# Kernel tuning notes

Measured on AMD Instinct MI355X. Metric: run time of the kernel, lower is better.

## Reference

```python
import jax, jax.numpy as jnp
import numpy as np

NA, NPAP = 50000, 100000
D_IN, D_HID, D_OUT = 512, 512, 256
E_AP, E_PA, E_AA = 400000, 400000, 200000
NEG_SLOPE = 0.2


def setup_inputs() -> dict:
    key = jax.random.key(0)
    ks = jax.random.split(key, 18)
    f32 = jnp.float32

    def edges(k, e, n_src, n_dst):
        k1, k2 = jax.random.split(k)
        return jnp.stack([
            jax.random.randint(k1, (e,), 0, n_src),
            jax.random.randint(k2, (e,), 0, n_dst),
        ]).astype(jnp.int64)

    return {
        'x_author': jax.random.normal(ks[0], (NA, D_IN), f32),
        'x_paper': jax.random.normal(ks[1], (NPAP, D_IN), f32),
        # layer 1 params
        'W1': jax.random.normal(ks[2], (2, D_IN, D_HID), f32) / np.sqrt(D_IN),
        'b1': jnp.zeros((2, D_HID), f32),
        'att1': jax.random.normal(ks[3], (3, 2, D_HID), f32) * 0.1,
        'kW1': jax.random.normal(ks[4], (D_HID, D_HID), f32) / np.sqrt(D_HID),
        'kb1': jnp.zeros((D_HID,), f32),
        'q1': jax.random.normal(ks[5], (D_HID,), f32) * 0.1,
        # layer 2 params
        'W2': jax.random.normal(ks[6], (2, D_HID, D_OUT), f32) / np.sqrt(D_HID),
        'b2': jnp.zeros((2, D_OUT), f32),
        'att2': jax.random.normal(ks[7], (3, 2, D_OUT), f32) * 0.1,
        'kW2': jax.random.normal(ks[8], (D_OUT, D_OUT), f32) / np.sqrt(D_OUT),
        'kb2': jnp.zeros((D_OUT,), f32),
        'q2': jax.random.normal(ks[9], (D_OUT,), f32) * 0.1,
        # edge index dict: (author,writes,paper), (paper,written_by,author), (author,coauthor,author)
        'e_ap': edges(ks[10], E_AP, NA, NPAP),
        'e_pa': edges(ks[11], E_PA, NPAP, NA),
        'e_aa': edges(ks[12], E_AA, NA, NA),
    }


def _edge_type_attn(h_src, h_dst, a_src, a_dst, ei, n_dst):
    """One edge-type GAT-style aggregation of HANConv (heads=1)."""
    src, dst = ei[0], ei[1]
    alpha = (h_src @ a_src)[src] + (h_dst @ a_dst)[dst]        # [E]
    alpha = jax.nn.leaky_relu(alpha, NEG_SLOPE)
    m = jax.ops.segment_max(alpha, dst, num_segments=n_dst)    # softmax over dst groups
    e = jnp.exp(alpha - m[dst])
    denom = jax.ops.segment_sum(e, dst, num_segments=n_dst)
    w = e / denom[dst]                                          # [E]
    out = jax.ops.segment_sum(h_src[src] * w[:, None], dst, num_segments=n_dst)
    return jax.nn.relu(out)                                     # [n_dst, D]


def _semantic_group(outs, kW, kb, q):
    """outs: [T, N, D]; semantic attention over T metapaths."""
    score = jnp.einsum('tnd,d->t', jnp.tanh(outs @ kW + kb), q) / outs.shape[1]
    attn = jax.nn.softmax(score)
    return jnp.einsum('t,tnd->nd', attn, outs)


def _han_layer(x_a, x_p, W, b, att, kW, kb, q, e_ap, e_pa, e_aa):
    h_a = x_a @ W[0] + b[0]   # per-node-type projection
    h_p = x_p @ W[1] + b[1]
    na, npap = h_a.shape[0], h_p.shape[0]
    out_p = _edge_type_attn(h_a, h_p, att[0, 0], att[0, 1], e_ap, npap)
    out_a1 = _edge_type_attn(h_p, h_a, att[1, 0], att[1, 1], e_pa, na)
    out_a2 = _edge_type_attn(h_a, h_a, att[2, 0], att[2, 1], e_aa, na)
    out_a = _semantic_group(jnp.stack([out_a1, out_a2]), kW, kb, q)
    out_p = _semantic_group(out_p[None], kW, kb, q)
    return out_a, out_p


def reference(x_author, x_paper, W1, b1, att1, kW1, kb1, q1,
              W2, b2, att2, kW2, kb2, q2, e_ap, e_pa, e_aa):
    h_a, h_p = _han_layer(x_author, x_paper, W1, b1, att1, kW1, kb1, q1, e_ap, e_pa, e_aa)
    h_a, h_p = _han_layer(h_a, h_p, W2, b2, att2, kW2, kb2, q2, e_ap, e_pa, e_aa)
    return h_a  # x['author']
```

## Files before the change

kernel.cpp:

```cpp
#include <hip/hip_runtime.h>
#include <hip/hip_bf16.h>

#define NA 50000
#define NPAP 100000
#define DIN 512
#define DHID 512
#define DOUT 256
#define EAP 400000
#define EPA 400000
#define EAA 200000

typedef unsigned short u16;
typedef __attribute__((ext_vector_type(8))) short bf16x8;
typedef __attribute__((ext_vector_type(4))) float f32x4;

__device__ inline float bflo(unsigned v) { return __uint_as_float(v << 16); }
__device__ inline float bfhi(unsigned v) { return __uint_as_float(v & 0xffff0000u); }
__device__ inline u16 f2bf_rne(float x) {
    unsigned u = __float_as_uint(x);
    return (u16)((u + 0x7FFFu + ((u >> 16) & 1u)) >> 16);
}
__device__ inline unsigned pack2bf(float a, float b) {
    return (unsigned)f2bf_rne(a) | ((unsigned)f2bf_rne(b) << 16);
}


__global__ void fill_u32_kernel(unsigned* __restrict__ p, unsigned v, int n) {
    int i = blockIdx.x * blockDim.x + threadIdx.x;
    if (i < n) p[i] = v;
}

__global__ void detect_kernel(const unsigned* __restrict__ e, int npairs, int* __restrict__ flag) {
    __shared__ int anyn;
    if (threadIdx.x == 0) anyn = 0;
    __syncthreads();
    unsigned local = 0;
    for (int i = threadIdx.x; i < npairs; i += blockDim.x) local |= e[2 * i + 1];
    if (local) atomicOr(&anyn, 1);
    __syncthreads();
    if (threadIdx.x == 0) flag[0] = (anyn == 0) ? 1 : 0;
}

__device__ inline int edge_at(const void* e, size_t idx, int i64) {
    return i64 ? (int)((const long long*)e)[idx] : ((const int*)e)[idx];
}


__global__ void conv_bt_kernel(const float* __restrict__ B, u16* __restrict__ bth,
                               u16* __restrict__ btl, int K, int N) {
    __shared__ float tile[32][33];
    const int nb = blockIdx.x * 32, kb = blockIdx.y * 32;
    const int tx = threadIdx.x, ty = threadIdx.y;
    const int KBLK = K >> 5;
    for (int i = ty; i < 32; i += 8)
        tile[i][tx] = B[(size_t)(kb + i) * N + nb + tx];
    __syncthreads();
    for (int i = ty; i < 32; i += 8) {
        float v = tile[tx][i];
        unsigned u = __float_as_uint(v);
        unsigned h = (u + 0x7FFFu + ((u >> 16) & 1u)) >> 16;
        float hf = __uint_as_float(h << 16);
        float r = v - hf;
        unsigned l = __float_as_uint(r) >> 16;
        const int n = nb + i, k = kb + tx;
        const int nblk = n >> 7, row = n & 127;
        const int kblk = k >> 5, kc = (k & 31) >> 3, ke = k & 7;
        const int cph = kc ^ ((row >> 1) & 3);
        size_t o = (((size_t)(nblk * KBLK + kblk) * 128 + row) << 5) + (cph << 3) + ke;
        bth[o] = (u16)h;
        btl[o] = (u16)l;
    }
}


template <bool BF16OUT>
__global__ __launch_bounds__(256, 4) void mfma_gemm_2p_kernel(
    const float* __restrict__ A,
    const u16* __restrict__ Bth, const u16* __restrict__ Btl,
    const float* __restrict__ bias,
    float* __restrict__ C, int M, int N, int K, int gx)
{
    __shared__ u16 Ah[128][32];
    __shared__ u16 Bh[128][32];
    __shared__ u16 Bl[128][32];

    const int nwg = gridDim.x;
    const int bid = blockIdx.x;
    const int qc = nwg >> 3, rc = nwg & 7;
    const int xcd = bid & 7, idx = bid >> 3;
    const int wg = (xcd < rc ? xcd * (qc + 1) : rc * (qc + 1) + (xcd - rc) * qc) + idx;
    const int bx = wg % gx, by = wg / gx;
    const int m0 = by * 128;
    const int n0 = bx * 128;

    const int tid = threadIdx.x;
    const int lane = tid & 63;
    const int wv = tid >> 6;
    const int wm = wv >> 1, wn = wv & 1;
    const int fr = lane & 15;
    const int kg = lane >> 4;

    const int srow = tid >> 1;
    const int oh   = tid & 1;
    const bool a_ok = (m0 + srow) < M;
    const float* Ap = A + (size_t)(m0 + srow) * K + oh * 16;

    const int swc = (srow >> 1) & 3;
    const int p0 = srow * 32 + ((((oh << 1) + 0) ^ swc) << 3);
    const int p1 = srow * 32 + ((((oh << 1) + 1) ^ swc) << 3);
    const int rdc = (kg ^ ((fr >> 1) & 3)) << 3;

    const int KBLK = K >> 5;
    const size_t btile0 = ((size_t)(n0 >> 7) * KBLK) << 12;
    const int bso0 = wv * 512 + lane * 8;
    const int bso1 = (wv + 4) * 512 + lane * 8;

    f32x4 acc[4][4] = {};

    const int nt = K >> 5;
    for (int t = 0; t < nt; ++t) {
        __syncthreads();
        {
            const int k0 = t << 5;
            uint4 w0 = make_uint4(0, 0, 0, 0), w1 = w0;
            if (a_ok) {
                float ar[16];
#pragma unroll
                for (int c4 = 0; c4 < 4; ++c4) {
                    float4 v = *(const float4*)(Ap + k0 + c4 * 4);
                    ar[c4 * 4 + 0] = v.x; ar[c4 * 4 + 1] = v.y;
                    ar[c4 * 4 + 2] = v.z; ar[c4 * 4 + 3] = v.w;
                }
                w0 = make_uint4(pack2bf(ar[0], ar[1]), pack2bf(ar[2], ar[3]),
                                pack2bf(ar[4], ar[5]), pack2bf(ar[6], ar[7]));
                w1 = make_uint4(pack2bf(ar[8], ar[9]), pack2bf(ar[10], ar[11]),
                                pack2bf(ar[12], ar[13]), pack2bf(ar[14], ar[15]));
            }
            const u16* bt = Bth + btile0 + ((size_t)t << 12);
            const u16* blt = Btl + btile0 + ((size_t)t << 12);
            uint4 bh0 = *(const uint4*)(bt + bso0);
            uint4 bh1 = *(const uint4*)(bt + bso1);
            uint4 bl0 = *(const uint4*)(blt + bso0);
            uint4 bl1 = *(const uint4*)(blt + bso1);

            u16* ahp = &Ah[0][0];
            *(uint4*)&ahp[p0] = w0;
            *(uint4*)&ahp[p1] = w1;
            u16* bhp = &Bh[0][0];
            u16* blp = &Bl[0][0];
            *(uint4*)&bhp[bso0] = bh0;
            *(uint4*)&bhp[bso1] = bh1;
            *(uint4*)&blp[bso0] = bl0;
            *(uint4*)&blp[bso1] = bl1;
        }
        __syncthreads();

        bf16x8 afh[4], bfh[4], bfl[4];
#pragma unroll
        for (int i = 0; i < 4; ++i) {
            const int aoff = (wm * 64 + i * 16 + fr) * 32 + rdc;
            const int boff = (wn * 64 + i * 16 + fr) * 32 + rdc;
            afh[i] = *(const bf16x8*)&Ah[0][aoff];
            bfh[i] = *(const bf16x8*)&Bh[0][boff];
            bfl[i] = *(const bf16x8*)&Bl[0][boff];
        }
#pragma unroll
        for (int i = 0; i < 4; ++i)
#pragma unroll
            for (int j = 0; j < 4; ++j) {
                acc[i][j] = __builtin_amdgcn_mfma_f32_16x16x32_bf16(afh[i], bfh[j], acc[i][j], 0, 0, 0);
                acc[i][j] = __builtin_amdgcn_mfma_f32_16x16x32_bf16(afh[i], bfl[j], acc[i][j], 0, 0, 0);
            }
    }

#pragma unroll
    for (int j = 0; j < 4; ++j) {
        const int col = n0 + wn * 64 + j * 16 + fr;
        const float bj = bias[col];
#pragma unroll
        for (int i = 0; i < 4; ++i) {
            const int rbase = m0 + wm * 64 + i * 16 + kg * 4;
#pragma unroll
            for (int r = 0; r < 4; ++r) {
                const int grow = rbase + r;
                if (grow < M) {
                    if (BF16OUT)
                        ((u16*)C)[(size_t)grow * N + col] = f2bf_rne(acc[i][j][r] + bj);
                    else
                        C[(size_t)grow * N + col] = acc[i][j][r] + bj;
                }
            }
        }
    }
}


template <bool COMB>
__global__ __launch_bounds__(256, 4) void mfma_gemm_bfA_kernel(
    const u16* __restrict__ A, const u16* __restrict__ A2,
    const float* __restrict__ cwp,
    const u16* __restrict__ Bth, const u16* __restrict__ Btl,
    const float* __restrict__ bias,
    float* __restrict__ C, int M, int N, int K, int gx)
{
    __shared__ u16 Ah[128][32];
    __shared__ u16 Bh[128][32];
    __shared__ u16 Bl[128][32];

    const int nwg = gridDim.x;
    const int bid = blockIdx.x;
    const int qc = nwg >> 3, rc = nwg & 7;
    const int xcd = bid & 7, idx = bid >> 3;
    const int wg = (xcd < rc ? xcd * (qc + 1) : rc * (qc + 1) + (xcd - rc) * qc) + idx;
    const int bx = wg % gx, by = wg / gx;
    const int m0 = by * 128;
    const int n0 = bx * 128;

    const int tid = threadIdx.x;
    const int lane = tid & 63;
    const int wv = tid >> 6;
    const int wm = wv >> 1, wn = wv & 1;
    const int fr = lane & 15;
    const int kg = lane >> 4;

    const int srow = tid >> 1;
    const int oh   = tid & 1;
    const bool a_ok = (m0 + srow) < M;
    const u16* Ap  = A + (size_t)(m0 + srow) * K + oh * 16;
    const u16* Ap2 = COMB ? (A2 + (size_t)(m0 + srow) * K + oh * 16) : nullptr;
    float cw0 = 1.f, cw1 = 0.f;
    if (COMB) { cw0 = cwp[0]; cw1 = cwp[1]; }

    const int swc = (srow >> 1) & 3;
    const int p0 = srow * 32 + ((((oh << 1) + 0) ^ swc) << 3);
    const int p1 = srow * 32 + ((((oh << 1) + 1) ^ swc) << 3);
    const int rdc = (kg ^ ((fr >> 1) & 3)) << 3;

    const int KBLK = K >> 5;
    const size_t btile0 = ((size_t)(n0 >> 7) * KBLK) << 12;
    const int bso0 = wv * 512 + lane * 8;
    const int bso1 = (wv + 4) * 512 + lane * 8;

    f32x4 acc[4][4] = {};

    const int nt = K >> 5;
    for (int t = 0; t < nt; ++t) {
        __syncthreads();
        {
            const int k0 = t << 5;
            uint4 a0 = make_uint4(0, 0, 0, 0), a1 = a0;
            if (a_ok) {
                a0 = *(const uint4*)(Ap + k0);
                a1 = *(const uint4*)(Ap + k0 + 8);
                if (COMB) {
                    uint4 c0 = *(const uint4*)(Ap2 + k0);
                    uint4 c1 = *(const uint4*)(Ap2 + k0 + 8);
                    a0.x = pack2bf(cw0 * bflo(a0.x) + cw1 * bflo(c0.x), cw0 * bfhi(a0.x) + cw1 * bfhi(c0.x));
                    a0.y = pack2bf(cw0 * bflo(a0.y) + cw1 * bflo(c0.y), cw0 * bfhi(a0.y) + cw1 * bfhi(c0.y));
                    a0.z = pack2bf(cw0 * bflo(a0.z) + cw1 * bflo(c0.z), cw0 * bfhi(a0.z) + cw1 * bfhi(c0.z));
                    a0.w = pack2bf(cw0 * bflo(a0.w) + cw1 * bflo(c0.w), cw0 * bfhi(a0.w) + cw1 * bfhi(c0.w));
                    a1.x = pack2bf(cw0 * bflo(a1.x) + cw1 * bflo(c1.x), cw0 * bfhi(a1.x) + cw1 * bfhi(c1.x));
                    a1.y = pack2bf(cw0 * bflo(a1.y) + cw1 * bflo(c1.y), cw0 * bfhi(a1.y) + cw1 * bfhi(c1.y));
                    a1.z = pack2bf(cw0 * bflo(a1.z) + cw1 * bflo(c1.z), cw0 * bfhi(a1.z) + cw1 * bfhi(c1.z));
                    a1.w = pack2bf(cw0 * bflo(a1.w) + cw1 * bflo(c1.w), cw0 * bfhi(a1.w) + cw1 * bfhi(c1.w));
                }
            }
            const u16* bt = Bth + btile0 + ((size_t)t << 12);
            const u16* blt = Btl + btile0 + ((size_t)t << 12);
            uint4 bh0 = *(const uint4*)(bt + bso0);
            uint4 bh1 = *(const uint4*)(bt + bso1);
            uint4 bl0 = *(const uint4*)(blt + bso0);
            uint4 bl1 = *(const uint4*)(blt + bso1);

            u16* ahp = &Ah[0][0];
            *(uint4*)&ahp[p0] = a0;
            *(uint4*)&ahp[p1] = a1;
            u16* bhp = &Bh[0][0];
            u16* blp = &Bl[0][0];
            *(uint4*)&bhp[bso0] = bh0;
            *(uint4*)&bhp[bso1] = bh1;
            *(uint4*)&blp[bso0] = bl0;
            *(uint4*)&blp[bso1] = bl1;
        }
        __syncthreads();

        bf16x8 afh[4], bfh[4], bfl[4];
#pragma unroll
        for (int i = 0; i < 4; ++i) {
            const int aoff = (wm * 64 + i * 16 + fr) * 32 + rdc;
            const int boff = (wn * 64 + i * 16 + fr) * 32 + rdc;
            afh[i] = *(const bf16x8*)&Ah[0][aoff];
            bfh[i] = *(const bf16x8*)&Bh[0][boff];
            bfl[i] = *(const bf16x8*)&Bl[0][boff];
        }
#pragma unroll
        for (int i = 0; i < 4; ++i)
#pragma unroll
            for (int j = 0; j < 4; ++j) {
                acc[i][j] = __builtin_amdgcn_mfma_f32_16x16x32_bf16(afh[i], bfh[j], acc[i][j], 0, 0, 0);
                acc[i][j] = __builtin_amdgcn_mfma_f32_16x16x32_bf16(afh[i], bfl[j], acc[i][j], 0, 0, 0);
            }
    }

#pragma unroll
    for (int j = 0; j < 4; ++j) {
        const int col = n0 + wn * 64 + j * 16 + fr;
        const float bj = bias[col];
#pragma unroll
        for (int i = 0; i < 4; ++i) {
            const int rbase = m0 + wm * 64 + i * 16 + kg * 4;
#pragma unroll
            for (int r = 0; r < 4; ++r) {
                const int grow = rbase + r;
                if (grow < M) C[(size_t)grow * N + col] = acc[i][j][r] + bj;
            }
        }
    }
}


template <bool BF16A>
__global__ __launch_bounds__(256, 4) void mfma_score1_kernel(
    const void* __restrict__ A_, const u16* __restrict__ Bth,
    const float* __restrict__ bias, int M, int N, int K,
    const float* __restrict__ qv, float* __restrict__ score, int gx)
{
    __shared__ u16 Ah[128][32];
    __shared__ u16 Bh[128][32];

    const int nwg = gridDim.x;
    const int bid = blockIdx.x;
    const int qc = nwg >> 3, rc = nwg & 7;
    const int xcd = bid & 7, idx = bid >> 3;
    const int wg = (xcd < rc ? xcd * (qc + 1) : rc * (qc + 1) + (xcd - rc) * qc) + idx;
    const int bx = wg % gx, by = wg / gx;
    const int m0 = by * 128;
    const int n0 = bx * 128;

    const int tid = threadIdx.x;
    const int lane = tid & 63;
    const int wv = tid >> 6;
    const int wm = wv >> 1, wn = wv & 1;
    const int fr = lane & 15;
    const int kg = lane >> 4;

    const int srow = tid >> 1;
    const int oh   = tid & 1;
    const bool a_ok = (m0 + srow) < M;

    const int swc = (srow >> 1) & 3;
    const int p0 = srow * 32 + ((((oh << 1) + 0) ^ swc) << 3);
    const int p1 = srow * 32 + ((((oh << 1) + 1) ^ swc) << 3);
    const int rdc = (kg ^ ((fr >> 1) & 3)) << 3;

    const int KBLK = K >> 5;
    const size_t btile0 = ((size_t)(n0 >> 7) * KBLK) << 12;
    const int bso0 = wv * 512 + lane * 8;
    const int bso1 = (wv + 4) * 512 + lane * 8;

    f32x4 acc[4][4] = {};

    const int nt = K >> 5;
    for (int t = 0; t < nt; ++t) {
        __syncthreads();
        {
            const int k0 = t << 5;
            uint4 w0 = make_uint4(0, 0, 0, 0), w1 = w0;
            if (a_ok) {
                if (BF16A) {
                    const u16* Ap = (const u16*)A_ + (size_t)(m0 + srow) * K + oh * 16;
                    w0 = *(const uint4*)(Ap + k0);
                    w1 = *(const uint4*)(Ap + k0 + 8);
                } else {
                    const float* Ap = (const float*)A_ + (size_t)(m0 + srow) * K + oh * 16;
                    float ar[16];
#pragma unroll
                    for (int c4 = 0; c4 < 4; ++c4) {
                        float4 v = *(const float4*)(Ap + k0 + c4 * 4);
                        ar[c4 * 4 + 0] = v.x; ar[c4 * 4 + 1] = v.y;
                        ar[c4 * 4 + 2] = v.z; ar[c4 * 4 + 3] = v.w;
                    }
                    w0 = make_uint4(pack2bf(ar[0], ar[1]), pack2bf(ar[2], ar[3]),
                                    pack2bf(ar[4], ar[5]), pack2bf(ar[6], ar[7]));
                    w1 = make_uint4(pack2bf(ar[8], ar[9]), pack2bf(ar[10], ar[11]),
                                    pack2bf(ar[12], ar[13]), pack2bf(ar[14], ar[15]));
                }
            }
            const u16* bt = Bth + btile0 + ((size_t)t << 12);
            uint4 bh0 = *(const uint4*)(bt + bso0);
            uint4 bh1 = *(const uint4*)(bt + bso1);
            u16* ahp = &Ah[0][0];
            *(uint4*)&ahp[p0] = w0;
            *(uint4*)&ahp[p1] = w1;
            u16* bhp = &Bh[0][0];
            *(uint4*)&bhp[bso0] = bh0;
            *(uint4*)&bhp[bso1] = bh1;
        }
        __syncthreads();

        bf16x8 afh[4], bfh[4];
#pragma unroll
        for (int i = 0; i < 4; ++i) {
            afh[i] = *(const bf16x8*)&Ah[0][(wm * 64 + i * 16 + fr) * 32 + rdc];
            bfh[i] = *(const bf16x8*)&Bh[0][(wn * 64 + i * 16 + fr) * 32 + rdc];
        }
#pragma unroll
        for (int i = 0; i < 4; ++i)
#pragma unroll
            for (int j = 0; j < 4; ++j)
                acc[i][j] = __builtin_amdgcn_mfma_f32_16x16x32_bf16(afh[i], bfh[j], acc[i][j], 0, 0, 0);
    }

    float ssum = 0.f;
#pragma unroll
    for (int j = 0; j < 4; ++j) {
        const int col = n0 + wn * 64 + j * 16 + fr;
        const float bj = bias[col];
        const float qj = qv[col];
#pragma unroll
        for (int i = 0; i < 4; ++i) {
            const int rbase = m0 + wm * 64 + i * 16 + kg * 4;
#pragma unroll
            for (int r = 0; r < 4; ++r) {
                if (rbase + r < M) ssum += tanhf(acc[i][j][r] + bj) * qj;
            }
        }
    }
#pragma unroll
    for (int o = 32; o; o >>= 1) ssum += __shfl_xor(ssum, o);
    __syncthreads();
    float* red = (float*)&Ah[0][0];
    if (lane == 0) red[wv] = ssum;
    __syncthreads();
    if (tid == 0) atomicAdd(score, red[0] + red[1] + red[2] + red[3]);
}


template <int NV, bool BF16IN>
__global__ void scores_kernel(const void* __restrict__ h, int n, int D,
                              const float* __restrict__ v0, const float* __restrict__ v1,
                              const float* __restrict__ v2, const float* __restrict__ v3,
                              float* __restrict__ s0, float* __restrict__ s1,
                              float* __restrict__ s2, float* __restrict__ s3)
{
    const int lane = threadIdx.x & 63;
    int wid = (blockIdx.x * blockDim.x + threadIdx.x) >> 6;
    const int nw = (gridDim.x * blockDim.x) >> 6;
    for (int node = wid; node < n; node += nw) {
        float a0 = 0, a1 = 0, a2 = 0, a3 = 0;
        for (int d = lane * 4; d < D; d += 256) {
            float4 x;
            if (BF16IN) {
                const u16* row = (const u16*)h + (size_t)node * D;
                uint2 bv = *(const uint2*)&row[d];
                x = make_float4(bflo(bv.x), bfhi(bv.x), bflo(bv.y), bfhi(bv.y));
            } else {
                const float* row = (const float*)h + (size_t)node * D;
                x = *(const float4*)&row[d];
            }
            float4 w = *(const float4*)&v0[d];
            a0 += x.x * w.x + x.y * w.y + x.z * w.z + x.w * w.w;
            if (NV > 1) { float4 u = *(const float4*)&v1[d]; a1 += x.x * u.x + x.y * u.y + x.z * u.z + x.w * u.w; }
            if (NV > 2) { float4 u = *(const float4*)&v2[d]; a2 += x.x * u.x + x.y * u.y + x.z * u.z + x.w * u.w; }
            if (NV > 3) { float4 u = *(const float4*)&v3[d]; a3 += x.x * u.x + x.y * u.y + x.z * u.z + x.w * u.w; }
        }
#pragma unroll
        for (int o = 32; o; o >>= 1) {
            a0 += __shfl_xor(a0, o);
            if (NV > 1) a1 += __shfl_xor(a1, o);
            if (NV > 2) a2 += __shfl_xor(a2, o);
            if (NV > 3) a3 += __shfl_xor(a3, o);
        }
        if (lane == 0) {
            s0[node] = a0;
            if (NV > 1) s1[node] = a1;
            if (NV > 2) s2[node] = a2;
            if (NV > 3) s3[node] = a3;
        }
    }
}


__global__ void count3_kernel(const void* __restrict__ eA, const void* __restrict__ eB,
                              const void* __restrict__ eC, const int* __restrict__ flag,
                              int* __restrict__ cA, int* __restrict__ cB, int* __restrict__ cC) {
    int i = blockIdx.x * blockDim.x + threadIdx.x;
    int f = *flag;
    if (i < EAP) {
        atomicAdd(&cA[edge_at(eA, (size_t)EAP + i, f)], 1);
    } else if (i < EAP + EPA) {
        int j = i - EAP;
        atomicAdd(&cB[edge_at(eB, (size_t)EPA + j, f)], 1);
    } else if (i < EAP + EPA + EAA) {
        int j = i - EAP - EPA;
        atomicAdd(&cC[edge_at(eC, (size_t)EAA + j, f)], 1);
    }
}

__global__ void scan3_kernel(int* __restrict__ c0, int n0_, int* __restrict__ o0, int* __restrict__ u0,
                             int* __restrict__ c1, int n1_, int* __restrict__ o1, int* __restrict__ u1,
                             int* __restrict__ c2, int n2_, int* __restrict__ o2, int* __restrict__ u2) {
    const int b = blockIdx.x;
    int* cnt   = b == 0 ? c0 : (b == 1 ? c1 : c2);
    const int n = b == 0 ? n0_ : (b == 1 ? n1_ : n2_);
    int* offs  = b == 0 ? o0 : (b == 1 ? o1 : o2);
    int* cur   = b == 0 ? u0 : (b == 1 ? u1 : u2);
    __shared__ int wsum[16];
    __shared__ int carry_s;
    const int t = threadIdx.x;
    const int lane = t & 63, w = t >> 6;
    if (t == 0) carry_s = 0;
    __syncthreads();
    for (int base = 0; base < n; base += 1024) {
        int v = (base + t < n) ? cnt[base + t] : 0;
        int x = v;
#pragma unroll
        for (int o = 1; o < 64; o <<= 1) {
            int y = __shfl_up(x, o);
            if (lane >= o) x += y;
        }
        if (lane == 63) wsum[w] = x;
        __syncthreads();
        if (w == 0 && lane < 16) {
            int s = wsum[lane];
#pragma unroll
            for (int o = 1; o < 16; o <<= 1) {
                int y = __shfl_up(s, o);
                if (lane >= o) s += y;
            }
            wsum[lane] = s;
        }
        __syncthreads();
        const int carry = carry_s;
        const int woff = (w > 0) ? wsum[w - 1] : 0;
        if (base + t < n) {
            int excl = carry + woff + x - v;
            offs[base + t] = excl;
            cur[base + t] = excl;
        }
        __syncthreads();
        if (t == 1023) carry_s = carry + wsum[15];
        __syncthreads();
    }
    if (t == 0) offs[n] = carry_s;
}

__global__ void scatter3_kernel(const void* __restrict__ eA, const void* __restrict__ eB,
                                const void* __restrict__ eC, const int* __restrict__ flag,
                                int* __restrict__ uA, int* __restrict__ uB, int* __restrict__ uC,
                                int* __restrict__ idA, int* __restrict__ idB, int* __restrict__ idC) {
    int i = blockIdx.x * blockDim.x + threadIdx.x;
    int f = *flag;
    if (i < EAP) {
        int d = edge_at(eA, (size_t)EAP + i, f);
        idA[atomicAdd(&uA[d], 1)] = i;
    } else if (i < EAP + EPA) {
        int j = i - EAP;
        int d = edge_at(eB, (size_t)EPA + j, f);
        idB[atomicAdd(&uB[d], 1)] = j;
    } else if (i < EAP + EPA + EAA) {
        int j = i - EAP - EPA;
        int d = edge_at(eC, (size_t)EAA + j, f);
        idC[atomicAdd(&uC[d], 1)] = j;
    }
}


template <int DW, bool BF16H, bool BF16OUT>
__global__ __launch_bounds__(256) void agg_fused_kernel(
    const int* __restrict__ offs, const int* __restrict__ eids,
    const void* __restrict__ e, const int* __restrict__ flag,
    const float* __restrict__ ssrc, const float* __restrict__ sdst,
    const void* __restrict__ hsrc_, void* __restrict__ out,
    int n_dst, int E, int D)
{
    const int lane = threadIdx.x & 63;
    int wid = (blockIdx.x * blockDim.x + threadIdx.x) >> 6;
    const int nw = (gridDim.x * blockDim.x) >> 6;
    const int f = *flag;
    for (int dst = wid; dst < n_dst; dst += nw) {
        const int beg = offs[dst], end = offs[dst + 1];
        const float sd = sdst[dst];

        float dsum = 0.f;
        for (int j = beg + lane; j < end; j += 64) {
            int eid = eids[j];
            float a = ssrc[edge_at(e, eid, f)] + sd;
            a = (a >= 0.f) ? a : 0.2f * a;
            dsum += expf(a);
        }
#pragma unroll
        for (int o = 32; o; o >>= 1) dsum += __shfl_xor(dsum, o);
        const float rden = (end > beg) ? 1.f / dsum : 0.f;

        float acc[DW] = {};
        int j = beg;
        for (; j + 4 <= end; j += 4) {
            const int e0 = eids[j], e1 = eids[j + 1], e2 = eids[j + 2], e3 = eids[j + 3];
            const int q0 = edge_at(e, e0, f), q1 = edge_at(e, e1, f);
            const int q2 = edge_at(e, e2, f), q3 = edge_at(e, e3, f);
            float a0 = ssrc[q0] + sd, a1 = ssrc[q1] + sd;
            float a2 = ssrc[q2] + sd, a3 = ssrc[q3] + sd;
            a0 = (a0 >= 0.f) ? a0 : 0.2f * a0;
            a1 = (a1 >= 0.f) ? a1 : 0.2f * a1;
            a2 = (a2 >= 0.f) ? a2 : 0.2f * a2;
            a3 = (a3 >= 0.f) ? a3 : 0.2f * a3;
            const float w0 = expf(a0) * rden, w1 = expf(a1) * rden;
            const float w2 = expf(a2) * rden, w3 = expf(a3) * rden;
            if (BF16H) {
                const u16* hb = (const u16*)hsrc_;
                const u16* r0 = hb + (size_t)q0 * D + lane * DW;
                const u16* r1 = hb + (size_t)q1 * D + lane * DW;
                const u16* r2 = hb + (size_t)q2 * D + lane * DW;
                const u16* r3 = hb + (size_t)q3 * D + lane * DW;
#pragma unroll
                for (int c = 0; c < DW; c += 8) {
                    uint4 b0 = *(const uint4*)&r0[c];
                    uint4 b1 = *(const uint4*)&r1[c];
                    uint4 b2 = *(const uint4*)&r2[c];
                    uint4 b3 = *(const uint4*)&r3[c];
                    acc[c + 0] += bflo(b0.x) * w0 + bflo(b1.x) * w1 + bflo(b2.x) * w2 + bflo(b3.x) * w3;
                    acc[c + 1] += bfhi(b0.x) * w0 + bfhi(b1.x) * w1 + bfhi(b2.x) * w2 + bfhi(b3.x) * w3;
                    acc[c + 2] += bflo(b0.y) * w0 + bflo(b1.y) * w1 + bflo(b2.y) * w2 + bflo(b3.y) * w3;
                    acc[c + 3] += bfhi(b0.y) * w0 + bfhi(b1.y) * w1 + bfhi(b2.y) * w2 + bfhi(b3.y) * w3;
                    acc[c + 4] += bflo(b0.z) * w0 + bflo(b1.z) * w1 + bflo(b2.z) * w2 + bflo(b3.z) * w3;
                    acc[c + 5] += bfhi(b0.z) * w0 + bfhi(b1.z) * w1 + bfhi(b2.z) * w2 + bfhi(b3.z) * w3;
                    acc[c + 6] += bflo(b0.w) * w0 + bflo(b1.w) * w1 + bflo(b2.w) * w2 + bflo(b3.w) * w3;
                    acc[c + 7] += bfhi(b0.w) * w0 + bfhi(b1.w) * w1 + bfhi(b2.w) * w2 + bfhi(b3.w) * w3;
                }
            } else {
                const float* hf = (const float*)hsrc_;
                const float* r0 = hf + (size_t)q0 * D + lane * DW;
                const float* r1 = hf + (size_t)q1 * D + lane * DW;
                const float* r2 = hf + (size_t)q2 * D + lane * DW;
                const float* r3 = hf + (size_t)q3 * D + lane * DW;
#pragma unroll
                for (int c = 0; c < DW; c += 4) {
                    float4 a0v = *(const float4*)&r0[c];
                    float4 a1v = *(const float4*)&r1[c];
                    float4 a2v = *(const float4*)&r2[c];
                    float4 a3v = *(const float4*)&r3[c];
                    acc[c + 0] += a0v.x * w0 + a1v.x * w1 + a2v.x * w2 + a3v.x * w3;
                    acc[c + 1] += a0v.y * w0 + a1v.y * w1 + a2v.y * w2 + a3v.y * w3;
                    acc[c + 2] += a0v.z * w0 + a1v.z * w1 + a2v.z * w2 + a3v.z * w3;
                    acc[c + 3] += a0v.w * w0 + a1v.w * w1 + a2v.w * w2 + a3v.w * w3;
                }
            }
        }
        for (; j < end; ++j) {
            const int eid = eids[j];
            const int q = edge_at(e, eid, f);
            float a = ssrc[q] + sd;
            a = (a >= 0.f) ? a : 0.2f * a;
            const float w = expf(a) * rden;
            if (BF16H) {
                const u16* row = (const u16*)hsrc_ + (size_t)q * D + lane * DW;
#pragma unroll
                for (int c = 0; c < DW; c += 8) {
                    uint4 b0 = *(const uint4*)&row[c];
                    acc[c + 0] += bflo(b0.x) * w; acc[c + 1] += bfhi(b0.x) * w;
                    acc[c + 2] += bflo(b0.y) * w; acc[c + 3] += bfhi(b0.y) * w;
                    acc[c + 4] += bflo(b0.z) * w; acc[c + 5] += bfhi(b0.z) * w;
                    acc[c + 6] += bflo(b0.w) * w; acc[c + 7] += bfhi(b0.w) * w;
                }
            } else {
                const float* row = (const float*)hsrc_ + (size_t)q * D + lane * DW;
#pragma unroll
                for (int c = 0; c < DW; c += 4) {
                    float4 v = *(const float4*)&row[c];
                    acc[c + 0] += v.x * w; acc[c + 1] += v.y * w;
                    acc[c + 2] += v.z * w; acc[c + 3] += v.w * w;
                }
            }
        }
        if (BF16OUT) {
            u16* orow = (u16*)out + (size_t)dst * D + lane * DW;
#pragma unroll
            for (int c = 0; c < DW; c += 8) {
                uint4 v;
                v.x = pack2bf(fmaxf(acc[c + 0], 0.f), fmaxf(acc[c + 1], 0.f));
                v.y = pack2bf(fmaxf(acc[c + 2], 0.f), fmaxf(acc[c + 3], 0.f));
                v.z = pack2bf(fmaxf(acc[c + 4], 0.f), fmaxf(acc[c + 5], 0.f));
                v.w = pack2bf(fmaxf(acc[c + 6], 0.f), fmaxf(acc[c + 7], 0.f));
                *(uint4*)&orow[c] = v;
            }
        } else {
            float* orow = (float*)out + (size_t)dst * D + lane * DW;
#pragma unroll
            for (int c = 0; c < DW; c += 4) {
                float4 v = make_float4(fmaxf(acc[c + 0], 0.f), fmaxf(acc[c + 1], 0.f),
                                       fmaxf(acc[c + 2], 0.f), fmaxf(acc[c + 3], 0.f));
                *(float4*)&orow[c] = v;
            }
        }
    }
}


__global__ void softmax2_kernel(const float* __restrict__ score, float invN, float* __restrict__ w) {
    if (threadIdx.x == 0 && blockIdx.x == 0) {
        float s0 = score[0] * invN, s1 = score[1] * invN;
        float m = fmaxf(s0, s1);
        float e0 = expf(s0 - m), e1 = expf(s1 - m);
        float r = 1.f / (e0 + e1);
        w[0] = e0 * r;
        w[1] = e1 * r;
    }
}

__global__ void combine2_kernel(const float4* __restrict__ a, const float4* __restrict__ b,
                                const float* __restrict__ w, float4* __restrict__ o, int n4) {
    float w0 = w[0], w1 = w[1];
    for (int i = blockIdx.x * blockDim.x + threadIdx.x; i < n4; i += gridDim.x * blockDim.x) {
        float4 x = a[i], y = b[i];
        o[i] = make_float4(w0 * x.x + w1 * y.x, w0 * x.y + w1 * y.y,
                           w0 * x.z + w1 * y.z, w0 * x.w + w1 * y.w);
    }
}


extern "C" void kernel_launch(void* const* d_in, const int* in_sizes, int n_in,
                              void* d_out, int out_size, void* d_ws, size_t ws_size,
                              hipStream_t stream) {
    const float* x_a  = (const float*)d_in[0];
    const float* x_p  = (const float*)d_in[1];
    const float* W1   = (const float*)d_in[2];
    const float* b1   = (const float*)d_in[3];
    const float* att1 = (const float*)d_in[4];
    const float* kW1  = (const float*)d_in[5];
    const float* kb1  = (const float*)d_in[6];
    const float* q1   = (const float*)d_in[7];
    const float* W2   = (const float*)d_in[8];
    const float* b2   = (const float*)d_in[9];
    const float* att2 = (const float*)d_in[10];
    const float* kW2  = (const float*)d_in[11];
    const float* kb2  = (const float*)d_in[12];
    const float* q2   = (const float*)d_in[13];
    const void* e_ap  = d_in[14];
    const void* e_pa  = d_in[15];
    const void* e_aa  = d_in[16];
    float* out = (float*)d_out;

    size_t off = 0;
    auto ALLOC = [&](size_t nbytes) -> void* {
        void* p = (char*)d_ws + off;
        off += (nbytes + 255) & ~(size_t)255;
        return p;
    };
    float* bufA = (float*)ALLOC((size_t)NPAP * DHID * 4);
    float* bufB = (float*)ALLOC((size_t)NA * DHID * 4);
    float* bufC = (float*)ALLOC((size_t)NA * DHID * 4);
    float* bufD = (float*)ALLOC((size_t)NA * DHID * 4);
    float* sa_w  = (float*)ALLOC((size_t)NA * 4);
    float* sa_pd = (float*)ALLOC((size_t)NA * 4);
    float* sa_as = (float*)ALLOC((size_t)NA * 4);
    float* sa_ad = (float*)ALLOC((size_t)NA * 4);
    float* sp_wd = (float*)ALLOC((size_t)NPAP * 4);
    float* sp_ps = (float*)ALLOC((size_t)NPAP * 4);
    int* cnt3    = (int*)ALLOC((size_t)(NPAP + 2 * NA + 8) * 4);
    int* cursor3 = (int*)ALLOC((size_t)(NPAP + 2 * NA + 8) * 4);
    int* offs_ap = (int*)ALLOC((size_t)(NPAP + 1) * 4);
    int* offs_pa = (int*)ALLOC((size_t)(NA + 1) * 4);
    int* offs_aa = (int*)ALLOC((size_t)(NA + 1) * 4);
    int* eids_ap = (int*)ALLOC((size_t)EAP * 4);
    int* eids_pa = (int*)ALLOC((size_t)EPA * 4);
    int* eids_aa = (int*)ALLOC((size_t)EAA * 4);
    const size_t WTOT = 262144u * 3 + 131072u * 2 + 65536u;
    u16* w_hi = (u16*)ALLOC(WTOT * 2);
    u16* w_lo = (u16*)ALLOC(WTOT * 2);
    float* score = (float*)ALLOC(8 * 4);
    float* wsem  = (float*)ALLOC(2 * 4);
    int* eflag   = (int*)ALLOC(4);
    if (off > ws_size) return;

    const size_t oW1a = 0, oW1p = 262144, okW1 = 524288;
    const size_t oW2a = 786432, oW2p = 917504, okW2 = 1048576;

    int* cntA = cnt3;                 int* curA = cursor3;
    int* cntB = cnt3 + NPAP + 1;      int* curB = cursor3 + NPAP + 1;
    int* cntC = cntB + NA + 1;        int* curC = curB + NA + 1;
    const int CNT3N = NPAP + 2 * NA + 3;

    hipStream_t s = stream;

    detect_kernel<<<1, 256, 0, s>>>((const unsigned*)e_ap, 1024, eflag);

    auto conv_b = [&](const float* B_, int K, int N, size_t wo) {
        conv_bt_kernel<<<dim3(N / 32, K / 32), dim3(32, 8), 0, s>>>(B_, w_hi + wo, w_lo + wo, K, N);
    };
    conv_b(W1, DIN, DHID, oW1a);
    conv_b(W1 + (size_t)DIN * DHID, DIN, DHID, oW1p);
    conv_b(kW1, DHID, DHID, okW1);
    conv_b(W2, DHID, DOUT, oW2a);
    conv_b(W2 + (size_t)DHID * DOUT, DHID, DOUT, oW2p);
    conv_b(kW2, DOUT, DOUT, okW2);

    {
        const int ETOT = EAP + EPA + EAA;
        fill_u32_kernel<<<(CNT3N + 255) / 256, 256, 0, s>>>((unsigned*)cnt3, 0u, CNT3N);
        count3_kernel<<<(ETOT + 255) / 256, 256, 0, s>>>(e_ap, e_pa, e_aa, eflag, cntA, cntB, cntC);
        scan3_kernel<<<3, 1024, 0, s>>>(cntA, NPAP, offs_ap, curA,
                                        cntB, NA, offs_pa, curB,
                                        cntC, NA, offs_aa, curC);
        scatter3_kernel<<<(ETOT + 255) / 256, 256, 0, s>>>(e_ap, e_pa, e_aa, eflag,
                                                           curA, curB, curC,
                                                           eids_ap, eids_pa, eids_aa);
    }

    auto gemm_proj_h = [&](const float* A_, size_t wo, const float* bias_, float* C_,
                           int M, int N, int K) {
        int gx = N / 128;
        int nwg = gx * ((M + 127) / 128);
        mfma_gemm_2p_kernel<true><<<nwg, 256, 0, s>>>(A_,
            w_hi + wo, w_lo + wo, bias_, C_, M, N, K, gx);
    };
    auto gemm_proj_bfA = [&](const u16* A_, size_t wo, const float* bias_, float* C_,
                             int M, int N, int K) {
        int gx = N / 128;
        int nwg = gx * ((M + 127) / 128);
        mfma_gemm_bfA_kernel<false><<<nwg, 256, 0, s>>>(A_, nullptr, nullptr,
            w_hi + wo, w_lo + wo, bias_, C_, M, N, K, gx);
    };
    auto gemm_proj_bfA_comb = [&](const u16* A_, const u16* A2_, const float* cw, size_t wo,
                                  const float* bias_, float* C_, int M, int N, int K) {
        int gx = N / 128;
        int nwg = gx * ((M + 127) / 128);
        mfma_gemm_bfA_kernel<true><<<nwg, 256, 0, s>>>(A_, A2_, cw,
            w_hi + wo, w_lo + wo, bias_, C_, M, N, K, gx);
    };
    auto gemm_score_b = [&](const void* A_, size_t wo, const float* bias_, int M, int N, int K,
                            const float* qv, float* sc) {
        int gx = N / 128;
        int nwg = gx * ((M + 127) / 128);
        mfma_score1_kernel<true><<<nwg, 256, 0, s>>>(A_, w_hi + wo, bias_, M, N, K, qv, sc, gx);
    };
    auto gemm_score_f = [&](const void* A_, size_t wo, const float* bias_, int M, int N, int K,
                            const float* qv, float* sc) {
        int gx = N / 128;
        int nwg = gx * ((M + 127) / 128);
        mfma_score1_kernel<false><<<nwg, 256, 0, s>>>(A_, w_hi + wo, bias_, M, N, K, qv, sc, gx);
    };

    u16* h_a = (u16*)bufB;
    u16* h_p = (u16*)bufA;
    gemm_proj_h(x_a, oW1a, b1, (float*)h_a, NA, DHID, DIN);
    gemm_proj_h(x_p, oW1p, b1 + DHID, (float*)h_p, NPAP, DHID, DIN);

    {
        int ga = (NA + 3) / 4 < 4096 ? (NA + 3) / 4 : 4096;
        int gp = (NPAP + 3) / 4 < 4096 ? (NPAP + 3) / 4 : 4096;
        scores_kernel<4, true><<<ga, 256, 0, s>>>(h_a, NA, DHID,
            att1 + 0 * DHID, att1 + 3 * DHID, att1 + 4 * DHID, att1 + 5 * DHID,
            sa_w, sa_pd, sa_as, sa_ad);
        scores_kernel<2, true><<<gp, 256, 0, s>>>(h_p, NPAP, DHID,
            att1 + 1 * DHID, att1 + 2 * DHID, nullptr, nullptr,
            sp_wd, sp_ps, nullptr, nullptr);
    }

    u16* o1  = (u16*)bufC;
    u16* o2  = (u16*)bufD;
    u16* x2p = (u16*)bufA + (size_t)NPAP * DHID;
    {
        int gw = (NA + 3) / 4;
        agg_fused_kernel<8, true, true><<<gw, 256, 0, s>>>(offs_pa, eids_pa, e_pa, eflag,
            sp_ps, sa_pd, h_p, o1, NA, EPA, DHID);
        agg_fused_kernel<8, true, true><<<gw, 256, 0, s>>>(offs_aa, eids_aa, e_aa, eflag,
            sa_as, sa_ad, h_a, o2, NA, EAA, DHID);
        int gw2 = (NPAP + 3) / 4;
        agg_fused_kernel<8, true, true><<<gw2, 256, 0, s>>>(offs_ap, eids_ap, e_ap, eflag,
            sa_w, sp_wd, h_a, x2p, NPAP, EAP, DHID);
    }

    fill_u32_kernel<<<1, 64, 0, s>>>((unsigned*)score, 0u, 2);
    gemm_score_b(o1, okW1, kb1, NA, DHID, DHID, q1, &score[0]);
    gemm_score_b(o2, okW1, kb1, NA, DHID, DHID, q1, &score[1]);
    softmax2_kernel<<<1, 64, 0, s>>>(score, 1.f / (float)NA, wsem);

    float* h2a = bufB;
    float* h2p = bufD;
    gemm_proj_bfA_comb(o1, o2, wsem, oW2a, b2, h2a, NA, DOUT, DHID);
    gemm_proj_bfA(x2p, oW2p, b2 + DOUT, h2p, NPAP, DOUT, DHID);

    {
        int ga = (NA + 3) / 4 < 4096 ? (NA + 3) / 4 : 4096;
        int gp = (NPAP + 3) / 4 < 4096 ? (NPAP + 3) / 4 : 4096;
        scores_kernel<3, false><<<ga, 256, 0, s>>>(h2a, NA, DOUT,
            att2 + 3 * DOUT, att2 + 4 * DOUT, att2 + 5 * DOUT, nullptr,
            sa_pd, sa_as, sa_ad, nullptr);
        scores_kernel<1, false><<<gp, 256, 0, s>>>(h2p, NPAP, DOUT,
            att2 + 2 * DOUT, nullptr, nullptr, nullptr,
            sp_ps, nullptr, nullptr, nullptr);
    }

    float* oa1 = bufC;
    float* oa2 = bufC + (size_t)NA * DOUT;
    {
        int gw = (NA + 3) / 4;
        agg_fused_kernel<4, false, false><<<gw, 256, 0, s>>>(offs_pa, eids_pa, e_pa, eflag,
            sp_ps, sa_pd, h2p, oa1, NA, EPA, DOUT);
        agg_fused_kernel<4, false, false><<<gw, 256, 0, s>>>(offs_aa, eids_aa, e_aa, eflag,
            sa_as, sa_ad, h2a, oa2, NA, EAA, DOUT);
    }

    fill_u32_kernel<<<1, 64, 0, s>>>((unsigned*)score, 0u, 2);
    gemm_score_f(oa1, okW2, kb2, NA, DOUT, DOUT, q2, &score[0]);
    gemm_score_f(oa2, okW2, kb2, NA, DOUT, DOUT, q2, &score[1]);
    softmax2_kernel<<<1, 64, 0, s>>>(score, 1.f / (float)NA, wsem);
    combine2_kernel<<<2048, 256, 0, s>>>((const float4*)oa1, (const float4*)oa2, wsem,
                                         (float4*)out, NA * DOUT / 4);
}
```

Before: 1.346 ms.

## Store layer-2 projections in bf16 and parallelize CSR offset scan

The layer-2 projection GEMMs now write bf16 instead of fp32, and the score and aggregation kernels read bf16 rows (a new DW=4 path using uint2 loads). This halves gather traffic in the second-layer edge aggregation and the projection write bandwidth, at the cost of extra rounding of the layer-2 features. Separately, the three-block sequential scan is replaced by a three-kernel multi-block scan over the concatenated count array, with offsets then rebased per edge type.

After: 1.242 ms (median of 2 runs). -7.8%, faster.

```diff
diff --git a/kernel.cpp b/kernel.cpp
--- a/kernel.cpp
+++ b/kernel.cpp
@@ -195,7 +195,7 @@
 }
 
 
-template <bool COMB>
+template <bool COMB, bool BF16OUT>
 __global__ __launch_bounds__(256, 4) void mfma_gemm_bfA_kernel(
     const u16* __restrict__ A, const u16* __restrict__ A2,
     const float* __restrict__ cwp,
@@ -312,7 +312,12 @@
 #pragma unroll
             for (int r = 0; r < 4; ++r) {
                 const int grow = rbase + r;
-                if (grow < M) C[(size_t)grow * N + col] = acc[i][j][r] + bj;
+                if (grow < M) {
+                    if (BF16OUT)
+                        ((u16*)C)[(size_t)grow * N + col] = f2bf_rne(acc[i][j][r] + bj);
+                    else
+                        C[(size_t)grow * N + col] = acc[i][j][r] + bj;
+                }
             }
         }
     }
@@ -497,52 +502,75 @@
     }
 }
 
-__global__ void scan3_kernel(int* __restrict__ c0, int n0_, int* __restrict__ o0, int* __restrict__ u0,
-                             int* __restrict__ c1, int n1_, int* __restrict__ o1, int* __restrict__ u1,
-                             int* __restrict__ c2, int n2_, int* __restrict__ o2, int* __restrict__ u2) {
-    const int b = blockIdx.x;
-    int* cnt   = b == 0 ? c0 : (b == 1 ? c1 : c2);
-    const int n = b == 0 ? n0_ : (b == 1 ? n1_ : n2_);
-    int* offs  = b == 0 ? o0 : (b == 1 ? o1 : o2);
-    int* cur   = b == 0 ? u0 : (b == 1 ? u1 : u2);
+
+__global__ void scanp1_kernel(const int* __restrict__ cnt, int n, int* __restrict__ part) {
     __shared__ int wsum[16];
-    __shared__ int carry_s;
-    const int t = threadIdx.x;
-    const int lane = t & 63, w = t >> 6;
-    if (t == 0) carry_s = 0;
+    const int base = blockIdx.x * 1024;
+    const int t = threadIdx.x, lane = t & 63, w = t >> 6;
+    int v = (base + t < n) ? cnt[base + t] : 0;
+#pragma unroll
+    for (int o = 1; o < 64; o <<= 1) v += __shfl_xor(v, o);
+    if (lane == 0) wsum[w] = v;
     __syncthreads();
-    for (int base = 0; base < n; base += 1024) {
-        int v = (base + t < n) ? cnt[base + t] : 0;
-        int x = v;
-#pragma unroll
-        for (int o = 1; o < 64; o <<= 1) {
-            int y = __shfl_up(x, o);
-            if (lane >= o) x += y;
-        }
-        if (lane == 63) wsum[w] = x;
-        __syncthreads();
-        if (w == 0 && lane < 16) {
-            int s = wsum[lane];
-#pragma unroll
-            for (int o = 1; o < 16; o <<= 1) {
-                int y = __shfl_up(s, o);
-                if (lane >= o) s += y;
-            }
-            wsum[lane] = s;
-        }
-        __syncthreads();
-        const int carry = carry_s;
-        const int woff = (w > 0) ? wsum[w - 1] : 0;
-        if (base + t < n) {
-            int excl = carry + woff + x - v;
-            offs[base + t] = excl;
-            cur[base + t] = excl;
-        }
-        __syncthreads();
-        if (t == 1023) carry_s = carry + wsum[15];
-        __syncthreads();
-    }
-    if (t == 0) offs[n] = carry_s;
+    if (t == 0) {
+        int s = 0;
+#pragma unroll
+        for (int k = 0; k < 16; ++k) s += wsum[k];
+        part[blockIdx.x] = s;
+    }
+}
+
+__global__ void scanp2_kernel(int* __restrict__ part, int nblk) {
+    __shared__ int wsum[16];
+    const int t = threadIdx.x, lane = t & 63, w = t >> 6;
+    int v = (t < nblk) ? part[t] : 0;
+    int x = v;
+#pragma unroll
+    for (int o = 1; o < 64; o <<= 1) { int y = __shfl_up(x, o); if (lane >= o) x += y; }
+    if (lane == 63) wsum[w] = x;
+    __syncthreads();
+    if (w == 0 && lane < 16) {
+        int s = wsum[lane];
+#pragma unroll
+        for (int o = 1; o < 16; o <<= 1) { int y = __shfl_up(s, o); if (lane >= o) s += y; }
+        wsum[lane] = s;
+    }
+    __syncthreads();
+    const int woff = (w > 0) ? wsum[w - 1] : 0;
+    if (t < nblk) part[t] = woff + x - v;
+}
+
+__global__ void scanp3_kernel(const int* __restrict__ cnt, int n, const int* __restrict__ part,
+                              int* __restrict__ offs_ap, int* __restrict__ cur_ap,
+                              int* __restrict__ offs_pa, int* __restrict__ cur_pa,
+                              int* __restrict__ offs_aa, int* __restrict__ cur_aa) {
+    __shared__ int wsum[16];
+    const int base = blockIdx.x * 1024;
+    const int t = threadIdx.x, lane = t & 63, w = t >> 6;
+    int v = (base + t < n) ? cnt[base + t] : 0;
+    int x = v;
+#pragma unroll
+    for (int o = 1; o < 64; o <<= 1) { int y = __shfl_up(x, o); if (lane >= o) x += y; }
+    if (lane == 63) wsum[w] = x;
+    __syncthreads();
+    if (w == 0 && lane < 16) {
+        int s = wsum[lane];
+#pragma unroll
+        for (int o = 1; o < 16; o <<= 1) { int y = __shfl_up(s, o); if (lane >= o) s += y; }
+        wsum[lane] = s;
+    }
+    __syncthreads();
+    const int woff = (w > 0) ? wsum[w - 1] : 0;
+    const int g = part[blockIdx.x] + woff + x - v;
+    const int i = base + t;
+    if (i < n) {
+        if (i < NPAP)                 { offs_ap[i] = g; cur_ap[i] = g; }
+        else if (i == NPAP)           { offs_ap[NPAP] = g; }
+        else if (i < NPAP + 1 + NA)   { int j = i - NPAP - 1; int val = g - EAP; offs_pa[j] = val; cur_pa[j] = val; }
+        else if (i == NPAP + 1 + NA)  { offs_pa[NA] = g - EAP; }
+        else if (i < NPAP + 2 + 2*NA) { int j = i - NPAP - NA - 2; int val = g - EAP - EPA; offs_aa[j] = val; cur_aa[j] = val; }
+        else                          { offs_aa[NA] = g - EAP - EPA; }
+    }
 }
 
 __global__ void scatter3_kernel(const void* __restrict__ eA, const void* __restrict__ eB,
@@ -613,20 +641,31 @@
                 const u16* r1 = hb + (size_t)q1 * D + lane * DW;
                 const u16* r2 = hb + (size_t)q2 * D + lane * DW;
                 const u16* r3 = hb + (size_t)q3 * D + lane * DW;
-#pragma unroll
-                for (int c = 0; c < DW; c += 8) {
-                    uint4 b0 = *(const uint4*)&r0[c];
-                    uint4 b1 = *(const uint4*)&r1[c];
-                    uint4 b2 = *(const uint4*)&r2[c];
-                    uint4 b3 = *(const uint4*)&r3[c];
-                    acc[c + 0] += bflo(b0.x) * w0 + bflo(b1.x) * w1 + bflo(b2.x) * w2 + bflo(b3.x) * w3;
-                    acc[c + 1] += bfhi(b0.x) * w0 + bfhi(b1.x) * w1 + bfhi(b2.x) * w2 + bfhi(b3.x) * w3;
-                    acc[c + 2] += bflo(b0.y) * w0 + bflo(b1.y) * w1 + bflo(b2.y) * w2 + bflo(b3.y) * w3;
-                    acc[c + 3] += bfhi(b0.y) * w0 + bfhi(b1.y) * w1 + bfhi(b2.y) * w2 + bfhi(b3.y) * w3;
-                    acc[c + 4] += bflo(b0.z) * w0 + bflo(b1.z) * w1 + bflo(b2.z) * w2 + bflo(b3.z) * w3;
-                    acc[c + 5] += bfhi(b0.z) * w0 + bfhi(b1.z) * w1 + bfhi(b2.z) * w2 + bfhi(b3.z) * w3;
-                    acc[c + 6] += bflo(b0.w) * w0 + bflo(b1.w) * w1 + bflo(b2.w) * w2 + bflo(b3.w) * w3;
-                    acc[c + 7] += bfhi(b0.w) * w0 + bfhi(b1.w) * w1 + bfhi(b2.w) * w2 + bfhi(b3.w) * w3;
+                if constexpr (DW >= 8) {
+#pragma unroll
+                    for (int c = 0; c < DW; c += 8) {
+                        uint4 b0 = *(const uint4*)&r0[c];
+                        uint4 b1 = *(const uint4*)&r1[c];
+                        uint4 b2 = *(const uint4*)&r2[c];
+                        uint4 b3 = *(const uint4*)&r3[c];
+                        acc[c + 0] += bflo(b0.x) * w0 + bflo(b1.x) * w1 + bflo(b2.x) * w2 + bflo(b3.x) * w3;
+                        acc[c + 1] += bfhi(b0.x) * w0 + bfhi(b1.x) * w1 + bfhi(b2.x) * w2 + bfhi(b3.x) * w3;
+                        acc[c + 2] += bflo(b0.y) * w0 + bflo(b1.y) * w1 + bflo(b2.y) * w2 + bflo(b3.y) * w3;
+                        acc[c + 3] += bfhi(b0.y) * w0 + bfhi(b1.y) * w1 + bfhi(b2.y) * w2 + bfhi(b3.y) * w3;
+                        acc[c + 4] += bflo(b0.z) * w0 + bflo(b1.z) * w1 + bflo(b2.z) * w2 + bflo(b3.z) * w3;
+                        acc[c + 5] += bfhi(b0.z) * w0 + bfhi(b1.z) * w1 + bfhi(b2.z) * w2 + bfhi(b3.z) * w3;
+                        acc[c + 6] += bflo(b0.w) * w0 + bflo(b1.w) * w1 + bflo(b2.w) * w2 + bflo(b3.w) * w3;
+                        acc[c + 7] += bfhi(b0.w) * w0 + bfhi(b1.w) * w1 + bfhi(b2.w) * w2 + bfhi(b3.w) * w3;
+                    }
+                } else {
+                    uint2 b0 = *(const uint2*)r0;
+                    uint2 b1 = *(const uint2*)r1;
+                    uint2 b2 = *(const uint2*)r2;
+                    uint2 b3 = *(const uint2*)r3;
+                    acc[0] += bflo(b0.x) * w0 + bflo(b1.x) * w1 + bflo(b2.x) * w2 + bflo(b3.x) * w3;
+                    acc[1] += bfhi(b0.x) * w0 + bfhi(b1.x) * w1 + bfhi(b2.x) * w2 + bfhi(b3.x) * w3;
+                    acc[2] += bflo(b0.y) * w0 + bflo(b1.y) * w1 + bflo(b2.y) * w2 + bflo(b3.y) * w3;
+                    acc[3] += bfhi(b0.y) * w0 + bfhi(b1.y) * w1 + bfhi(b2.y) * w2 + bfhi(b3.y) * w3;
                 }
             } else {
                 const float* hf = (const float*)hsrc_;
@@ -655,13 +694,19 @@
             const float w = expf(a) * rden;
             if (BF16H) {
                 const u16* row = (const u16*)hsrc_ + (size_t)q * D + lane * DW;
-#pragma unroll
-                for (int c = 0; c < DW; c += 8) {
-                    uint4 b0 = *(const uint4*)&row[c];
-                    acc[c + 0] += bflo(b0.x) * w; acc[c + 1] += bfhi(b0.x) * w;
-                    acc[c + 2] += bflo(b0.y) * w; acc[c + 3] += bfhi(b0.y) * w;
-                    acc[c + 4] += bflo(b0.z) * w; acc[c + 5] += bfhi(b0.z) * w;
-                    acc[c + 6] += bflo(b0.w) * w; acc[c + 7] += bfhi(b0.w) * w;
+                if constexpr (DW >= 8) {
+#pragma unroll
+                    for (int c = 0; c < DW; c += 8) {
+                        uint4 b0 = *(const uint4*)&row[c];
+                        acc[c + 0] += bflo(b0.x) * w; acc[c + 1] += bfhi(b0.x) * w;
+                        acc[c + 2] += bflo(b0.y) * w; acc[c + 3] += bfhi(b0.y) * w;
+                        acc[c + 4] += bflo(b0.z) * w; acc[c + 5] += bfhi(b0.z) * w;
+                        acc[c + 6] += bflo(b0.w) * w; acc[c + 7] += bfhi(b0.w) * w;
+                    }
+                } else {
+                    uint2 b0 = *(const uint2*)row;
+                    acc[0] += bflo(b0.x) * w; acc[1] += bfhi(b0.x) * w;
+                    acc[2] += bflo(b0.y) * w; acc[3] += bfhi(b0.y) * w;
                 }
             } else {
                 const float* row = (const float*)hsrc_ + (size_t)q * D + lane * DW;
@@ -675,14 +720,21 @@
         }
         if (BF16OUT) {
             u16* orow = (u16*)out + (size_t)dst * D + lane * DW;
-#pragma unroll
-            for (int c = 0; c < DW; c += 8) {
-                uint4 v;
-                v.x = pack2bf(fmaxf(acc[c + 0], 0.f), fmaxf(acc[c + 1], 0.f));
-                v.y = pack2bf(fmaxf(acc[c + 2], 0.f), fmaxf(acc[c + 3], 0.f));
-                v.z = pack2bf(fmaxf(acc[c + 4], 0.f), fmaxf(acc[c + 5], 0.f));
-                v.w = pack2bf(fmaxf(acc[c + 6], 0.f), fmaxf(acc[c + 7], 0.f));
-                *(uint4*)&orow[c] = v;
+            if constexpr (DW >= 8) {
+#pragma unroll
+                for (int c = 0; c < DW; c += 8) {
+                    uint4 v;
+                    v.x = pack2bf(fmaxf(acc[c + 0], 0.f), fmaxf(acc[c + 1], 0.f));
+                    v.y = pack2bf(fmaxf(acc[c + 2], 0.f), fmaxf(acc[c + 3], 0.f));
+                    v.z = pack2bf(fmaxf(acc[c + 4], 0.f), fmaxf(acc[c + 5], 0.f));
+                    v.w = pack2bf(fmaxf(acc[c + 6], 0.f), fmaxf(acc[c + 7], 0.f));
+                    *(uint4*)&orow[c] = v;
+                }
+            } else {
+                uint2 v;
+                v.x = pack2bf(fmaxf(acc[0], 0.f), fmaxf(acc[1], 0.f));
+                v.y = pack2bf(fmaxf(acc[2], 0.f), fmaxf(acc[3], 0.f));
+                *(uint2*)orow = v;
             }
         } else {
             float* orow = (float*)out + (size_t)dst * D + lane * DW;
@@ -758,6 +810,7 @@
     float* sp_wd = (float*)ALLOC((size_t)NPAP * 4);
     float* sp_ps = (float*)ALLOC((size_t)NPAP * 4);
     int* cnt3    = (int*)ALLOC((size_t)(NPAP + 2 * NA + 8) * 4);
+    int* scanpart = (int*)ALLOC(256 * 4);
     int* cursor3 = (int*)ALLOC((size_t)(NPAP + 2 * NA + 8) * 4);
     int* offs_ap = (int*)ALLOC((size_t)(NPAP + 1) * 4);
     int* offs_pa = (int*)ALLOC((size_t)(NA + 1) * 4);
@@ -776,9 +829,12 @@
     const size_t oW1a = 0, oW1p = 262144, okW1 = 524288;
     const size_t oW2a = 786432, oW2p = 917504, okW2 = 1048576;
 
-    int* cntA = cnt3;                 int* curA = cursor3;
-    int* cntB = cnt3 + NPAP + 1;      int* curB = cursor3 + NPAP + 1;
-    int* cntC = cntB + NA + 1;        int* curC = curB + NA + 1;
+    int* cntA = cnt3;
+    int* cntB = cnt3 + NPAP + 1;
+    int* cntC = cntB + NA + 1;
+    int* curA = cursor3;
+    int* curB = cursor3 + NPAP + 1;
+    int* curC = curB + NA + 1;
     const int CNT3N = NPAP + 2 * NA + 3;
 
     hipStream_t s = stream;
@@ -797,11 +853,13 @@
 
     {
         const int ETOT = EAP + EPA + EAA;
+        const int nblk = (CNT3N + 1023) / 1024;
         fill_u32_kernel<<<(CNT3N + 255) / 256, 256, 0, s>>>((unsigned*)cnt3, 0u, CNT3N);
         count3_kernel<<<(ETOT + 255) / 256, 256, 0, s>>>(e_ap, e_pa, e_aa, eflag, cntA, cntB, cntC);
-        scan3_kernel<<<3, 1024, 0, s>>>(cntA, NPAP, offs_ap, curA,
-                                        cntB, NA, offs_pa, curB,
-                                        cntC, NA, offs_aa, curC);
+        scanp1_kernel<<<nblk, 1024, 0, s>>>(cnt3, CNT3N, scanpart);
+        scanp2_kernel<<<1, 1024, 0, s>>>(scanpart, nblk);
+        scanp3_kernel<<<nblk, 1024, 0, s>>>(cnt3, CNT3N, scanpart,
+                                            offs_ap, curA, offs_pa, curB, offs_aa, curC);
         scatter3_kernel<<<(ETOT + 255) / 256, 256, 0, s>>>(e_ap, e_pa, e_aa, eflag,
                                                            curA, curB, curC,
                                                            eids_ap, eids_pa, eids_aa);
@@ -814,18 +872,18 @@
         mfma_gemm_2p_kernel<true><<<nwg, 256, 0, s>>>(A_,
             w_hi + wo, w_lo + wo, bias_, C_, M, N, K, gx);
     };
-    auto gemm_proj_bfA = [&](const u16* A_, size_t wo, const float* bias_, float* C_,
-                             int M, int N, int K) {
+    auto gemm_proj_bfA_h = [&](const u16* A_, size_t wo, const float* bias_, float* C_,
+                               int M, int N, int K) {
         int gx = N / 128;
         int nwg = gx * ((M + 127) / 128);
-        mfma_gemm_bfA_kernel<false><<<nwg, 256, 0, s>>>(A_, nullptr, nullptr,
+        mfma_gemm_bfA_kernel<false, true><<<nwg, 256, 0, s>>>(A_, nullptr, nullptr,
             w_hi + wo, w_lo + wo, bias_, C_, M, N, K, gx);
     };
-    auto gemm_proj_bfA_comb = [&](const u16* A_, const u16* A2_, const float* cw, size_t wo,
-                                  const float* bias_, float* C_, int M, int N, int K) {
+    auto gemm_proj_bfA_comb_h = [&](const u16* A_, const u16* A2_, const float* cw, size_t wo,
+                                    const float* bias_, float* C_, int M, int N, int K) {
         int gx = N / 128;
         int nwg = gx * ((M + 127) / 128);
-        mfma_gemm_bfA_kernel<true><<<nwg, 256, 0, s>>>(A_, A2_, cw,
+        mfma_gemm_bfA_kernel<true, true><<<nwg, 256, 0, s>>>(A_, A2_, cw,
             w_hi + wo, w_lo + wo, bias_, C_, M, N, K, gx);
     };
     auto gemm_score_b = [&](const void* A_, size_t wo, const float* bias_, int M, int N, int K,
@@ -876,18 +934,18 @@
     gemm_score_b(o2, okW1, kb1, NA, DHID, DHID, q1, &score[1]);
     softmax2_kernel<<<1, 64, 0, s>>>(score, 1.f / (float)NA, wsem);
 
-    float* h2a = bufB;
-    float* h2p = bufD;
-    gemm_proj_bfA_comb(o1, o2, wsem, oW2a, b2, h2a, NA, DOUT, DHID);
-    gemm_proj_bfA(x2p, oW2p, b2 + DOUT, h2p, NPAP, DOUT, DHID);
+    u16* h2a = (u16*)bufB;
+    u16* h2p = (u16*)bufD;
+    gemm_proj_bfA_comb_h(o1, o2, wsem, oW2a, b2, (float*)h2a, NA, DOUT, DHID);
+    gemm_proj_bfA_h(x2p, oW2p, b2 + DOUT, (float*)h2p, NPAP, DOUT, DHID);
 
     {
         int ga = (NA + 3) / 4 < 4096 ? (NA + 3) / 4 : 4096;
         int gp = (NPAP + 3) / 4 < 4096 ? (NPAP + 3) / 4 : 4096;
-        scores_kernel<3, false><<<ga, 256, 0, s>>>(h2a, NA, DOUT,
+        scores_kernel<3, true><<<ga, 256, 0, s>>>(h2a, NA, DOUT,
             att2 + 3 * DOUT, att2 + 4 * DOUT, att2 + 5 * DOUT, nullptr,
             sa_pd, sa_as, sa_ad, nullptr);
-        scores_kernel<1, false><<<gp, 256, 0, s>>>(h2p, NPAP, DOUT,
+        scores_kernel<1, true><<<gp, 256, 0, s>>>(h2p, NPAP, DOUT,
             att2 + 2 * DOUT, nullptr, nullptr, nullptr,
             sp_ps, nullptr, nullptr, nullptr);
     }
@@ -896,9 +954,9 @@
     float* oa2 = bufC + (size_t)NA * DOUT;
     {
         int gw = (NA + 3) / 4;
-        agg_fused_kernel<4, false, false><<<gw, 256, 0, s>>>(offs_pa, eids_pa, e_pa, eflag,
+        agg_fused_kernel<4, true, false><<<gw, 256, 0, s>>>(offs_pa, eids_pa, e_pa, eflag,
             sp_ps, sa_pd, h2p, oa1, NA, EPA, DOUT);
-        agg_fused_kernel<4, false, false><<<gw, 256, 0, s>>>(offs_aa, eids_aa, e_aa, eflag,
+        agg_fused_kernel<4, true, false><<<gw, 256, 0, s>>>(offs_aa, eids_aa, e_aa, eflag,
             sa_as, sa_ad, h2a, oa2, NA, EAA, DOUT);
     }
 
```
